# Kernel optimization log

Hardware: AMD Instinct MI355X
Metric: run time of the kernel (lower is better)

## Reference

```python
import jax, jax.numpy as jnp
import numpy as np

# dims: B batch, T obs_length, NOV num_ov, N nodes, F feature size, NF node feat, EF edge feat
B, T, NOV, N, F, NF, EF = 32, 10, 3, 128, 16, 5, 2
C = NOV + 1      # c_size channels in GCN
SL = 2           # stack_length of gcn_module1 (repo default assumption)
HID = N * F      # critic/actor hidden


def setup_inputs() -> dict:
    key = jax.random.key(0)
    ks = jax.random.split(key, 20)
    s = 0.05
    return {
        "inputs": jax.random.uniform(ks[0], (B, T * NOV, N, 3 * N + NF), dtype=jnp.float32),
        "We": jax.random.normal(ks[1], (EF, F), dtype=jnp.float32) * s,
        "be": jax.random.normal(ks[2], (F,), dtype=jnp.float32) * s,
        "Wn": jax.random.normal(ks[3], (NF, F), dtype=jnp.float32) * s,
        "bn": jax.random.normal(ks[4], (F,), dtype=jnp.float32) * s,
        "Wg": jax.random.normal(ks[5], (SL, C, F, F), dtype=jnp.float32) * s,   # per-layer per-channel linear weights
        "bgl": jax.random.normal(ks[6], (SL, C, F), dtype=jnp.float32) * s,     # per-layer per-channel linear biases
        "gbias": jax.random.normal(ks[7], (C, 1, F), dtype=jnp.float32) * s,    # GNN_module.bias
        "Wc1": jax.random.normal(ks[8], (C * N * F, HID), dtype=jnp.float32) * s,
        "bc1": jax.random.normal(ks[9], (HID,), dtype=jnp.float32) * s,
        "Wc2": jax.random.normal(ks[10], (HID, F), dtype=jnp.float32) * s,
        "bc2": jax.random.normal(ks[11], (F,), dtype=jnp.float32) * s,
        "Wc3": jax.random.normal(ks[12], (F, 1), dtype=jnp.float32) * s,
        "bc3": jax.random.normal(ks[13], (1,), dtype=jnp.float32) * s,
        "Wa1": jax.random.normal(ks[14], (C * N * F, HID), dtype=jnp.float32) * s,
        "ba1": jax.random.normal(ks[15], (HID,), dtype=jnp.float32) * s,
        "Wa2": jax.random.normal(ks[16], (HID, F), dtype=jnp.float32) * s,
        "ba2": jax.random.normal(ks[17], (F,), dtype=jnp.float32) * s,
    }


def _gcn(adj, x, Wg, bgl, gbias):
    # adj: [M,N,N]; x: [M,C,N,F_in]. Faithful to GNN_module.forward with add_loop=True.
    n = adj.shape[1]
    i = jnp.arange(n)
    a = adj.at[:, i, i].set(1.0)  # self loops
    for l in range(Wg.shape[0]):
        c_in = x.shape[1]
        # lin_i(x).sum(dim=1) for each output channel i; bias summed over c_in channels
        y = jnp.einsum('bcnf,ifo->bino', x, Wg[l]) + c_in * bgl[l][None, :, None, :]
        # degree re-normalization each stack layer (as in original)
        deg = jnp.clip(a.sum(-1), 1.0) ** -0.5
        a = deg[:, :, None] * a * deg[:, None, :]
        x = jax.nn.leaky_relu(jnp.einsum('bnm,bcmo->bcno', a, y) + gbias)
    return x


def reference(inputs, We, be, Wn, bn, Wg, bgl, gbias,
              Wc1, bc1, Wc2, bc2, Wc3, bc3, Wa1, ba1, Wa2, ba2):
    b = inputs.shape[0]
    adj = inputs[:, 0, :, :N]                                   # [b,N,N]
    edge = inputs[:, 0, :, N:3 * N].reshape(b, N, N, EF)        # [b,N,N,2]
    node = inputs[:, :, :, 3 * N:].reshape(b, T, NOV, N, NF)    # [b,T,NOV,N,5]

    edge_enc = (jax.nn.leaky_relu(edge @ We + be) * adj[..., None]).sum(axis=1)  # [b,N,F]
    node_enc = jax.nn.leaky_relu(node @ Wn + bn)                                 # [b,T,NOV,N,F]

    # encode loop over t vectorized by folding t into batch
    feats = jnp.concatenate(
        [jnp.broadcast_to(edge_enc[:, None, None], (b, T, 1, N, F)), node_enc], axis=2
    )                                                            # [b,T,C,N,F]
    adj_rep = jnp.broadcast_to(adj[:, None], (b, T, N, N)).reshape(b * T, N, N)
    g = _gcn(adj_rep, feats.reshape(b * T, C, N, F), Wg, bgl, gbias)
    graph = g.reshape(b, T, C, N, F).sum(axis=1)                 # out accumulated over obs_length

    flat = graph.reshape(b, -1)                                  # [b, C*N*F]
    h = jax.nn.leaky_relu(flat @ Wc1 + bc1)
    h = jax.nn.leaky_relu(h @ Wc2 + bc2)
    critic = h @ Wc3 + bc3                                       # [b,1]
    ha = jax.nn.leaky_relu(flat @ Wa1 + ba1)
    actor = jax.nn.leaky_relu(ha @ Wa2 + ba2)                    # [b,F]
    return (critic, actor)
```

## Files before the change

kernel.cpp:

```cpp
#include <hip/hip_runtime.h>
#include <stdint.h>

#define LEAKY(x) ((x) > 0.f ? (x) : 0.01f*(x))

typedef __attribute__((ext_vector_type(8))) short bf16x8;
typedef __attribute__((ext_vector_type(4))) float f32x4;

__device__ __forceinline__ unsigned short f2bf(float x){
  unsigned u = __float_as_uint(x);
  u += 0x7FFFu + ((u >> 16) & 1u);
  return (unsigned short)(u >> 16);
}
__device__ __forceinline__ void fma4(float4& a, float s, const float4& w){
  a.x = fmaf(s, w.x, a.x); a.y = fmaf(s, w.y, a.y);
  a.z = fmaf(s, w.z, a.z); a.w = fmaf(s, w.w, a.w);
}
__device__ __forceinline__ float dot16(const float* __restrict__ xn, const float* wg, float a){
  float4 x0 = *(const float4*)(xn);
  float4 x1 = *(const float4*)(xn+4);
  float4 x2 = *(const float4*)(xn+8);
  float4 x3 = *(const float4*)(xn+12);
  a = fmaf(x0.x, wg[0], a);  a = fmaf(x0.y, wg[1], a);  a = fmaf(x0.z, wg[2], a);  a = fmaf(x0.w, wg[3], a);
  a = fmaf(x1.x, wg[4], a);  a = fmaf(x1.y, wg[5], a);  a = fmaf(x1.z, wg[6], a);  a = fmaf(x1.w, wg[7], a);
  a = fmaf(x2.x, wg[8], a);  a = fmaf(x2.y, wg[9], a);  a = fmaf(x2.z, wg[10], a); a = fmaf(x2.w, wg[11], a);
  a = fmaf(x3.x, wg[12], a); a = fmaf(x3.y, wg[13], a); a = fmaf(x3.z, wg[14], a); a = fmaf(x3.w, wg[15], a);
  return a;
}

__global__ __launch_bounds__(256) void k_stage1(const float* __restrict__ inp,
                                                const float* __restrict__ We,
                                                const float* __restrict__ be,
                                                const float* __restrict__ Wn,
                                                const float* __restrict__ bn,
                                                float* __restrict__ edge_enc,
                                                unsigned short* __restrict__ A1b,
                                                unsigned short* __restrict__ A2b,
                                                float* __restrict__ S){
  __shared__ float sm[16896];
  int bx = blockIdx.x, t = threadIdx.x;

  if (bx < 256){
    int b = bx >> 3, jg = bx & 7;
    int j = jg*16 + (t >> 4), f = t & 15;
    const float* base = inp + (size_t)b*30*128*389;
    float w0 = We[f], w1 = We[16+f], bf = be[f];
    float acc = 0.f;
    #pragma unroll 4
    for (int i = 0; i < 128; ++i){
      const float* row = base + i*389;
      float adjv = row[j];
      float2 e = *(const float2*)(row + 128 + 2*j);
      float v = fmaf(e.x, w0, fmaf(e.y, w1, bf));
      v = LEAKY(v);
      acc = fmaf(v, adjv, acc);
    }
    edge_enc[b*2048 + j*16 + f] = acc;
  } else if (bx < 288){
    float* As = sm; float* ps = sm + 16512; float* dg = sm + 16768;
    int b = bx - 256;
    const float* base = inp + (size_t)b*30*128*389;
    for (int idx = t; idx < 16384; idx += 256){
      int n = idx >> 7, m = idx & 127;
      As[n*129 + m] = base[n*389 + m];
    }
    __syncthreads();
    if (t < 128) As[t*129 + t] = 1.0f;
    __syncthreads();
    for (int pass = 0; pass < 2; ++pass){
      int n = t >> 1, h = t & 1;
      float s = 0.f;
      for (int m = h*64; m < h*64 + 64; ++m) s += As[n*129 + m];
      ps[t] = s;
      __syncthreads();
      if (t < 128) dg[t] = rsqrtf(fmaxf(ps[2*t] + ps[2*t+1], 1.0f));
      __syncthreads();
      unsigned short* dst = pass ? A2b : A1b;
      for (int idx = t; idx < 16384; idx += 256){
        int nn = idx >> 7, m = idx & 127;
        float v = dg[nn] * As[nn*129 + m] * dg[m];
        if (!pass) As[nn*129 + m] = v;
        dst[b*16384 + idx] = f2bf(v);
      }
      __syncthreads();
    }
  } else {
    float* WnL = sm; float* bnL = sm + 80;
    if (t < 80) WnL[t] = Wn[t];
    if (t < 16) bnL[t] = bn[t];
    __syncthreads();
    int id = (bx - 288)*256 + t;
    int b = id / 1280, rem = id % 1280;
    int tt = rem >> 7, n = rem & 127;
    float outv[16];
    #pragma unroll
    for (int f = 0; f < 16; ++f) outv[f] = 0.f;
    for (int v = 0; v < 3; ++v){
      const float* row = inp + (size_t)((b*30 + tt*3 + v)*128 + n)*389 + 384;
      float x0 = row[0], x1 = row[1], x2 = row[2], x3 = row[3], x4 = row[4];
      #pragma unroll
      for (int f = 0; f < 16; ++f){
        float a = bnL[f];
        a = fmaf(x0, WnL[f], a);
        a = fmaf(x1, WnL[16+f], a);
        a = fmaf(x2, WnL[32+f], a);
        a = fmaf(x3, WnL[48+f], a);
        a = fmaf(x4, WnL[64+f], a);
        outv[f] += LEAKY(a);
      }
    }
    float* dst = S + (size_t)((b*10 + tt)*128 + n)*16;
    #pragma unroll
    for (int q = 0; q < 4; ++q)
      *(float4*)(dst + q*4) = make_float4(outv[q*4], outv[q*4+1], outv[q*4+2], outv[q*4+3]);
  }
}

__global__ __launch_bounds__(256) void k_gcn(const float* __restrict__ edge_enc,
                                             const float* __restrict__ S,
                                             const unsigned short* __restrict__ A1b,
                                             const unsigned short* __restrict__ A2b,
                                             const float* __restrict__ Wg,
                                             const float* __restrict__ bgl,
                                             const float* __restrict__ gbias,
                                             float* __restrict__ g10){
  __shared__ __align__(16) unsigned short Af[128*136];
  __shared__ __align__(16) unsigned short YT[64*136];
  __shared__ __align__(16) float xsb[128*16];
  int blk = blockIdx.x;
  int b = blk/10, tt = blk%10;
  int t = threadIdx.x, lane = t & 63, wave = t >> 6;
  int io = lane, ic = io >> 4, o = io & 15;
  int lo = lane & 15, qd = lane >> 4;

  float wg0[16], wg1[16];
  #pragma unroll
  for (int f = 0; f < 16; ++f){
    wg0[f] = Wg[(ic*16 + f)*16 + o];
    wg1[f] = Wg[((4 + ic)*16 + f)*16 + o];
  }
  float bg0 = 4.f * bgl[ic*16 + o];
  float bg1 = 4.f * bgl[64 + ic*16 + o];
  float gb[4];
  #pragma unroll
  for (int q = 0; q < 4; ++q) gb[q] = gbias[q*16 + lo];

  uint4 areg[8];
  {
    const uint4* gA = (const uint4*)(A1b + b*16384);
    #pragma unroll
    for (int q = 0; q < 8; ++q) areg[q] = gA[q*256 + t];
  }
  {
    const float4* ge = (const float4*)(edge_enc + b*2048);
    const float4* gs = (const float4*)(S + (size_t)(b*10 + tt)*2048);
    float4* xf = (float4*)xsb;
    float4 a0 = ge[2*t], s0 = gs[2*t];
    float4 a1 = ge[2*t+1], s1 = gs[2*t+1];
    xf[2*t]   = make_float4(a0.x+s0.x, a0.y+s0.y, a0.z+s0.z, a0.w+s0.w);
    xf[2*t+1] = make_float4(a1.x+s1.x, a1.y+s1.y, a1.z+s1.z, a1.w+s1.w);
  }
  __syncthreads();

  #pragma unroll
  for (int nb = 0; nb < 32; nb += 8){
    unsigned pk[4];
    #pragma unroll
    for (int u = 0; u < 8; ++u){
      int n = wave*32 + nb + u;
      float a = dot16(&xsb[n*16], wg0, bg0);
      unsigned short hb = f2bf(a);
      if (u & 1) pk[u>>1] |= ((unsigned)hb) << 16; else pk[u>>1] = (unsigned)hb;
    }
    *(uint4*)&YT[io*136 + wave*32 + nb] = make_uint4(pk[0], pk[1], pk[2], pk[3]);
  }
  #pragma unroll
  for (int q = 0; q < 8; ++q){
    int c = q*256 + t;
    *(uint4*)&Af[(c >> 4)*136 + (c & 15)*8] = areg[q];
  }
  __syncthreads();

  f32x4 acc0[2][4];
  #pragma unroll
  for (int mi = 0; mi < 2; ++mi)
    #pragma unroll
    for (int nt = 0; nt < 4; ++nt) acc0[mi][nt] = (f32x4){0.f,0.f,0.f,0.f};
  #pragma unroll
  for (int kt = 0; kt < 4; ++kt){
    bf16x8 av[2], bv[4];
    #pragma unroll
    for (int mi = 0; mi < 2; ++mi)
      av[mi] = *(const bf16x8*)&Af[(wave*32 + mi*16 + lo)*136 + kt*32 + qd*8];
    #pragma unroll
    for (int nt = 0; nt < 4; ++nt)
      bv[nt] = *(const bf16x8*)&YT[(nt*16 + lo)*136 + kt*32 + qd*8];
    #pragma unroll
    for (int mi = 0; mi < 2; ++mi)
      #pragma unroll
      for (int nt = 0; nt < 4; ++nt)
        acc0[mi][nt] = __builtin_amdgcn_mfma_f32_16x16x32_bf16(av[mi], bv[nt], acc0[mi][nt], 0, 0, 0);
  }
  {
    const uint4* gA = (const uint4*)(A2b + b*16384);
    #pragma unroll
    for (int q = 0; q < 8; ++q) areg[q] = gA[q*256 + t];
  }
  #pragma unroll
  for (int mi = 0; mi < 2; ++mi)
    #pragma unroll
    for (int r = 0; r < 4; ++r){
      float s = 0.f;
      #pragma unroll
      for (int nt = 0; nt < 4; ++nt){
        float v = acc0[mi][nt][r] + gb[nt];
        s += LEAKY(v);
      }
      int n = wave*32 + mi*16 + qd*4 + r;
      xsb[n*16 + lo] = s;
    }
  __syncthreads();

  #pragma unroll
  for (int nb = 0; nb < 32; nb += 8){
    unsigned pk[4];
    #pragma unroll
    for (int u = 0; u < 8; ++u){
      int n = wave*32 + nb + u;
      float a = dot16(&xsb[n*16], wg1, bg1);
      unsigned short hb = f2bf(a);
      if (u & 1) pk[u>>1] |= ((unsigned)hb) << 16; else pk[u>>1] = (unsigned)hb;
    }
    *(uint4*)&YT[io*136 + wave*32 + nb] = make_uint4(pk[0], pk[1], pk[2], pk[3]);
  }
  #pragma unroll
  for (int q = 0; q < 8; ++q){
    int c = q*256 + t;
    *(uint4*)&Af[(c >> 4)*136 + (c & 15)*8] = areg[q];
  }
  __syncthreads();

  f32x4 acc1[2][4];
  #pragma unroll
  for (int mi = 0; mi < 2; ++mi)
    #pragma unroll
    for (int nt = 0; nt < 4; ++nt) acc1[mi][nt] = (f32x4){0.f,0.f,0.f,0.f};
  #pragma unroll
  for (int kt = 0; kt < 4; ++kt){
    bf16x8 av[2], bv[4];
    #pragma unroll
    for (int mi = 0; mi < 2; ++mi)
      av[mi] = *(const bf16x8*)&Af[(wave*32 + mi*16 + lo)*136 + kt*32 + qd*8];
    #pragma unroll
    for (int nt = 0; nt < 4; ++nt)
      bv[nt] = *(const bf16x8*)&YT[(nt*16 + lo)*136 + kt*32 + qd*8];
    #pragma unroll
    for (int mi = 0; mi < 2; ++mi)
      #pragma unroll
      for (int nt = 0; nt < 4; ++nt)
        acc1[mi][nt] = __builtin_amdgcn_mfma_f32_16x16x32_bf16(av[mi], bv[nt], acc1[mi][nt], 0, 0, 0);
  }
  float* gout = g10 + (size_t)(b*10 + tt)*8192;
  #pragma unroll
  for (int mi = 0; mi < 2; ++mi)
    #pragma unroll
    for (int nt = 0; nt < 4; ++nt)
      #pragma unroll
      for (int r = 0; r < 4; ++r){
        float v = acc1[mi][nt][r] + gb[nt];
        v = LEAKY(v);
        int n = wave*32 + mi*16 + qd*4 + r;
        gout[nt*2048 + n*16 + lo] = v;
      }
}

__global__ __launch_bounds__(256) void k_sum(const float* __restrict__ g10,
                                             float* __restrict__ graph){
  int blk = blockIdx.x;
  int b = blk >> 3, seg = blk & 7;
  int t = threadIdx.x;
  size_t off = (size_t)seg*1024 + t*4;
  float4 a = make_float4(0.f,0.f,0.f,0.f);
  #pragma unroll
  for (int tt = 0; tt < 10; ++tt){
    float4 v = *(const float4*)(g10 + (size_t)(b*10 + tt)*8192 + off);
    a.x += v.x; a.y += v.y; a.z += v.z; a.w += v.w;
  }
  *(float4*)(graph + (size_t)b*8192 + off) = a;
}

__global__ __launch_bounds__(256) void k_gemm(const float* __restrict__ graph,
                                              const float* __restrict__ Wc1,
                                              const float* __restrict__ Wa1,
                                              float* __restrict__ part){
  __shared__ __align__(16) float flatc[32*256];
  __shared__ __align__(16) float Wt[16*256];
  int bx = blockIdx.x;
  int ks = bx >> 4, cb = bx & 15;
  const float* W = (cb < 8) ? Wc1 : Wa1;
  int cw0 = (cb & 7) * 256;
  int k0 = ks * 256;
  int t = threadIdx.x, lane = t & 63, wave = t >> 6;
  #pragma unroll
  for (int q = 0; q < 8; ++q){
    int idx4 = t + 256*q; int r = idx4 >> 6, c4 = idx4 & 63;
    *(float4*)&flatc[r*256 + c4*4] = *(const float4*)(graph + (size_t)r*8192 + k0 + c4*4);
  }
  float4 acc4[8];
  #pragma unroll
  for (int i = 0; i < 8; ++i) acc4[i] = make_float4(0.f,0.f,0.f,0.f);
  float4 stg[4];
  #pragma unroll
  for (int q = 0; q < 4; ++q){
    int idx4 = t + 256*q; int s = idx4 >> 6, c4 = idx4 & 63;
    stg[q] = *(const float4*)(W + (size_t)(k0 + s)*2048 + cw0 + c4*4);
  }
  int r0 = wave*8, c0l = lane*4;
  for (int j = 0; j < 16; ++j){
    asm volatile("s_waitcnt lgkmcnt(0)\ns_barrier" ::: "memory");
    #pragma unroll
    for (int q = 0; q < 4; ++q){
      int idx4 = t + 256*q; int s = idx4 >> 6, c4 = idx4 & 63;
      *(float4*)&Wt[s*256 + c4*4] = stg[q];
    }
    if (j < 15){
      #pragma unroll
      for (int q = 0; q < 4; ++q){
        int idx4 = t + 256*q; int s = idx4 >> 6, c4 = idx4 & 63;
        stg[q] = *(const float4*)(W + (size_t)(k0 + (j+1)*16 + s)*2048 + cw0 + c4*4);
      }
    }
    asm volatile("s_waitcnt lgkmcnt(0)\ns_barrier" ::: "memory");
    #pragma unroll
    for (int kk4 = 0; kk4 < 4; ++kk4){
      float4 wv0 = *(const float4*)&Wt[(kk4*4+0)*256 + c0l];
      float4 wv1 = *(const float4*)&Wt[(kk4*4+1)*256 + c0l];
      float4 wv2 = *(const float4*)&Wt[(kk4*4+2)*256 + c0l];
      float4 wv3 = *(const float4*)&Wt[(kk4*4+3)*256 + c0l];
      #pragma unroll
      for (int ii = 0; ii < 8; ++ii){
        float4 fvv = *(const float4*)&flatc[(r0+ii)*256 + j*16 + kk4*4];
        fma4(acc4[ii], fvv.x, wv0);
        fma4(acc4[ii], fvv.y, wv1);
        fma4(acc4[ii], fvv.z, wv2);
        fma4(acc4[ii], fvv.w, wv3);
      }
    }
  }
  float* dst = part + (size_t)ks*131072 + cb*256 + c0l;
  #pragma unroll
  for (int ii = 0; ii < 8; ++ii)
    *(float4*)(dst + (size_t)(r0+ii)*4096) = acc4[ii];
}

__global__ __launch_bounds__(256) void k_heads(const float* __restrict__ part,
                                               const float* __restrict__ bc1,
                                               const float* __restrict__ ba1,
                                               const float* __restrict__ Wc2,
                                               const float* __restrict__ bc2,
                                               const float* __restrict__ Wc3,
                                               const float* __restrict__ bc3,
                                               const float* __restrict__ Wa2,
                                               const float* __restrict__ ba2,
                                               float* __restrict__ out){
  __shared__ float red[256*17];
  int r = blockIdx.x >> 1, which = blockIdx.x & 1;
  int t = threadIdx.x;
  const float* W2 = which ? Wa2 : Wc2;
  const float* b1 = which ? ba1 : bc1;
  const float* pbase = part + (size_t)r*4096 + which*2048;
  float acc[16];
  #pragma unroll
  for (int f = 0; f < 16; ++f) acc[f] = 0.f;
  for (int k = t; k < 2048; k += 256){
    float s = 0.f;
    #pragma unroll 8
    for (int p = 0; p < 32; ++p) s += pbase[(size_t)p*131072 + k];
    s += b1[k];
    float xv = LEAKY(s);
    const float4* wr = (const float4*)(W2 + k*16);
    float4 w0 = wr[0], w1 = wr[1], w2 = wr[2], w3 = wr[3];
    acc[0]  = fmaf(xv, w0.x, acc[0]);  acc[1]  = fmaf(xv, w0.y, acc[1]);
    acc[2]  = fmaf(xv, w0.z, acc[2]);  acc[3]  = fmaf(xv, w0.w, acc[3]);
    acc[4]  = fmaf(xv, w1.x, acc[4]);  acc[5]  = fmaf(xv, w1.y, acc[5]);
    acc[6]  = fmaf(xv, w1.z, acc[6]);  acc[7]  = fmaf(xv, w1.w, acc[7]);
    acc[8]  = fmaf(xv, w2.x, acc[8]);  acc[9]  = fmaf(xv, w2.y, acc[9]);
    acc[10] = fmaf(xv, w2.z, acc[10]); acc[11] = fmaf(xv, w2.w, acc[11]);
    acc[12] = fmaf(xv, w3.x, acc[12]); acc[13] = fmaf(xv, w3.y, acc[13]);
    acc[14] = fmaf(xv, w3.z, acc[14]); acc[15] = fmaf(xv, w3.w, acc[15]);
  }
  #pragma unroll
  for (int f = 0; f < 16; ++f) red[t*17 + f] = acc[f];
  __syncthreads();
  for (int off = 128; off >= 1; off >>= 1){
    if (t < off){
      #pragma unroll
      for (int f = 0; f < 16; ++f) red[t*17 + f] += red[(t+off)*17 + f];
    }
    __syncthreads();
  }
  if (which == 0){
    if (t == 0){
      float c = bc3[0];
      #pragma unroll
      for (int f = 0; f < 16; ++f){
        float v = red[f] + bc2[f];
        v = LEAKY(v);
        c = fmaf(v, Wc3[f], c);
      }
      out[r] = c;
    }
  } else {
    if (t < 16){
      float v = red[t] + ba2[t];
      out[32 + r*16 + t] = LEAKY(v);
    }
  }
}

static const size_t O_EDGE  = 0;
static const size_t O_S     = 262144;
static const size_t O_A1    = 2883584;
static const size_t O_A2    = 3932160;
static const size_t O_G10   = 4980736;
static const size_t O_GRAPH = 15466496;
static const size_t O_PART  = 16515072;

extern "C" void kernel_launch(void* const* d_in, const int* in_sizes, int n_in,
                              void* d_out, int out_size, void* d_ws, size_t ws_size,
                              hipStream_t stream){
  const float* inp  = (const float*)d_in[0];
  const float* We   = (const float*)d_in[1];
  const float* be   = (const float*)d_in[2];
  const float* Wn   = (const float*)d_in[3];
  const float* bn   = (const float*)d_in[4];
  const float* Wg   = (const float*)d_in[5];
  const float* bgl  = (const float*)d_in[6];
  const float* gbias= (const float*)d_in[7];
  const float* Wc1  = (const float*)d_in[8];
  const float* bc1  = (const float*)d_in[9];
  const float* Wc2  = (const float*)d_in[10];
  const float* bc2  = (const float*)d_in[11];
  const float* Wc3  = (const float*)d_in[12];
  const float* bc3  = (const float*)d_in[13];
  const float* Wa1  = (const float*)d_in[14];
  const float* ba1  = (const float*)d_in[15];
  const float* Wa2  = (const float*)d_in[16];
  const float* ba2  = (const float*)d_in[17];

  char* ws = (char*)d_ws;
  float* edge_enc      = (float*)(ws + O_EDGE);
  float* S             = (float*)(ws + O_S);
  unsigned short* A1b  = (unsigned short*)(ws + O_A1);
  unsigned short* A2b  = (unsigned short*)(ws + O_A2);
  float* g10           = (float*)(ws + O_G10);
  float* graph         = (float*)(ws + O_GRAPH);
  float* part          = (float*)(ws + O_PART);

  hipLaunchKernelGGL(k_stage1, dim3(448), dim3(256), 0, stream, inp, We, be, Wn, bn, edge_enc, A1b, A2b, S);
  hipLaunchKernelGGL(k_gcn,    dim3(320), dim3(256), 0, stream, edge_enc, S, A1b, A2b, Wg, bgl, gbias, g10);
  hipLaunchKernelGGL(k_sum,    dim3(256), dim3(256), 0, stream, g10, graph);
  hipLaunchKernelGGL(k_gemm,   dim3(512), dim3(256), 0, stream, graph, Wc1, Wa1, part);
  hipLaunchKernelGGL(k_heads,  dim3(64),  dim3(256), 0, stream, part, bc1, ba1, Wc2, bc2, Wc3, bc3, Wa2, ba2, (float*)d_out);
}
```

Before: 403.6 us.

## Split edge encoder reduction over row chunks with LDS staging and partial sums

The edge-encoding blocks now each handle a 16-row chunk of the adjacency/edge rows for one batch, rather than a 16-column slice across all 128 rows. Each block stages its chunk coalesced into shared memory and writes a per-chunk partial sum into an 8x larger buffer. The GCN kernel then sums the 8 partials when it builds its input features. The intent is to replace strided per-row global loads in the long serial loop with coalesced bulk loads and short reductions. The cost is extra workspace, more reads in k_gcn, and a shifted workspace layout.

```diff
diff --git a/kernel.cpp b/kernel.cpp
--- a/kernel.cpp
+++ b/kernel.cpp
@@ -32,7 +32,7 @@
                                                 const float* __restrict__ be,
                                                 const float* __restrict__ Wn,
                                                 const float* __restrict__ bn,
-                                                float* __restrict__ edge_enc,
+                                                float* __restrict__ edge8,
                                                 unsigned short* __restrict__ A1b,
                                                 unsigned short* __restrict__ A2b,
                                                 float* __restrict__ S){
@@ -40,21 +40,33 @@
   int bx = blockIdx.x, t = threadIdx.x;
 
   if (bx < 256){
-    int b = bx >> 3, jg = bx & 7;
-    int j = jg*16 + (t >> 4), f = t & 15;
-    const float* base = inp + (size_t)b*30*128*389;
+    int b = bx >> 3, ic = bx & 7;
+    const float* base = inp + ((size_t)b*30*128 + ic*16)*389;
+    #pragma unroll
+    for (int q = 0; q < 24; ++q){
+      int idx = q*256 + t;
+      int r = idx / 384, c = idx % 384;
+      sm[r*384 + c] = base[(size_t)r*389 + c];
+    }
+    __syncthreads();
+    int f = t & 15, jb = t >> 4;
     float w0 = We[f], w1 = We[16+f], bf = be[f];
-    float acc = 0.f;
-    #pragma unroll 4
-    for (int i = 0; i < 128; ++i){
-      const float* row = base + i*389;
-      float adjv = row[j];
-      float2 e = *(const float2*)(row + 128 + 2*j);
-      float v = fmaf(e.x, w0, fmaf(e.y, w1, bf));
-      v = LEAKY(v);
-      acc = fmaf(v, adjv, acc);
-    }
-    edge_enc[b*2048 + j*16 + f] = acc;
+    float* dst = edge8 + (size_t)(b*8 + ic)*2048;
+    #pragma unroll
+    for (int jj = 0; jj < 8; ++jj){
+      int j = jb + 16*jj;
+      float acc = 0.f;
+      #pragma unroll
+      for (int r = 0; r < 16; ++r){
+        float adjv = sm[r*384 + j];
+        float e0   = sm[r*384 + 128 + 2*j];
+        float e1   = sm[r*384 + 129 + 2*j];
+        float v = fmaf(e0, w0, fmaf(e1, w1, bf));
+        v = LEAKY(v);
+        acc = fmaf(v, adjv, acc);
+      }
+      dst[j*16 + f] = acc;
+    }
   } else if (bx < 288){
     float* As = sm; float* ps = sm + 16512; float* dg = sm + 16768;
     int b = bx - 256;
@@ -94,6 +106,7 @@
     float outv[16];
     #pragma unroll
     for (int f = 0; f < 16; ++f) outv[f] = 0.f;
+    #pragma unroll
     for (int v = 0; v < 3; ++v){
       const float* row = inp + (size_t)((b*30 + tt*3 + v)*128 + n)*389 + 384;
       float x0 = row[0], x1 = row[1], x2 = row[2], x3 = row[3], x4 = row[4];
@@ -115,7 +128,7 @@
   }
 }
 
-__global__ __launch_bounds__(256) void k_gcn(const float* __restrict__ edge_enc,
+__global__ __launch_bounds__(256) void k_gcn(const float* __restrict__ edge8,
                                              const float* __restrict__ S,
                                              const unsigned short* __restrict__ A1b,
                                              const unsigned short* __restrict__ A2b,
@@ -151,13 +164,17 @@
     for (int q = 0; q < 8; ++q) areg[q] = gA[q*256 + t];
   }
   {
-    const float4* ge = (const float4*)(edge_enc + b*2048);
+    const float4* ge = (const float4*)(edge8 + (size_t)b*8*2048);
     const float4* gs = (const float4*)(S + (size_t)(b*10 + tt)*2048);
+    float4 a0 = gs[2*t], a1 = gs[2*t+1];
+    #pragma unroll
+    for (int s = 0; s < 8; ++s){
+      float4 v0 = ge[s*512 + 2*t], v1 = ge[s*512 + 2*t + 1];
+      a0.x += v0.x; a0.y += v0.y; a0.z += v0.z; a0.w += v0.w;
+      a1.x += v1.x; a1.y += v1.y; a1.z += v1.z; a1.w += v1.w;
+    }
     float4* xf = (float4*)xsb;
-    float4 a0 = ge[2*t], s0 = gs[2*t];
-    float4 a1 = ge[2*t+1], s1 = gs[2*t+1];
-    xf[2*t]   = make_float4(a0.x+s0.x, a0.y+s0.y, a0.z+s0.z, a0.w+s0.w);
-    xf[2*t+1] = make_float4(a1.x+s1.x, a1.y+s1.y, a1.z+s1.z, a1.w+s1.w);
+    xf[2*t] = a0; xf[2*t+1] = a1;
   }
   __syncthreads();
 
@@ -417,13 +434,13 @@
   }
 }
 
-static const size_t O_EDGE  = 0;
-static const size_t O_S     = 262144;
-static const size_t O_A1    = 2883584;
-static const size_t O_A2    = 3932160;
-static const size_t O_G10   = 4980736;
-static const size_t O_GRAPH = 15466496;
-static const size_t O_PART  = 16515072;
+static const size_t O_EDGE8 = 0;
+static const size_t O_S     = 2097152;
+static const size_t O_A1    = 4718592;
+static const size_t O_A2    = 5767168;
+static const size_t O_G10   = 6815744;
+static const size_t O_GRAPH = 17301504;
+static const size_t O_PART  = 18350080;
 
 extern "C" void kernel_launch(void* const* d_in, const int* in_sizes, int n_in,
                               void* d_out, int out_size, void* d_ws, size_t ws_size,
@@ -448,7 +465,7 @@
   const float* ba2  = (const float*)d_in[17];
 
   char* ws = (char*)d_ws;
-  float* edge_enc      = (float*)(ws + O_EDGE);
+  float* edge8         = (float*)(ws + O_EDGE8);
   float* S             = (float*)(ws + O_S);
   unsigned short* A1b  = (unsigned short*)(ws + O_A1);
   unsigned short* A2b  = (unsigned short*)(ws + O_A2);
@@ -456,8 +473,8 @@
   float* graph         = (float*)(ws + O_GRAPH);
   float* part          = (float*)(ws + O_PART);
 
-  hipLaunchKernelGGL(k_stage1, dim3(448), dim3(256), 0, stream, inp, We, be, Wn, bn, edge_enc, A1b, A2b, S);
-  hipLaunchKernelGGL(k_gcn,    dim3(320), dim3(256), 0, stream, edge_enc, S, A1b, A2b, Wg, bgl, gbias, g10);
+  hipLaunchKernelGGL(k_stage1, dim3(448), dim3(256), 0, stream, inp, We, be, Wn, bn, edge8, A1b, A2b, S);
+  hipLaunchKernelGGL(k_gcn,    dim3(320), dim3(256), 0, stream, edge8, S, A1b, A2b, Wg, bgl, gbias, g10);
   hipLaunchKernelGGL(k_sum,    dim3(256), dim3(256), 0, stream, g10, graph);
   hipLaunchKernelGGL(k_gemm,   dim3(512), dim3(256), 0, stream, graph, Wc1, Wa1, part);
   hipLaunchKernelGGL(k_heads,  dim3(64),  dim3(256), 0, stream, part, bc1, ba1, Wc2, bc2, Wc3, bc3, Wa2, ba2, (float*)d_out);
```

Result: no change. 404.0 us (+0.1%).
